# Kernel tuning notes

Measured on AMD Instinct MI355X. Metric: run time of the kernel, lower is better.

The kernel has to match this reference:

```python
import jax, jax.numpy as jnp
import numpy as np

N = 100000       # nodes
E = 1600000      # edges (avg degree 16)
F_IN = 64        # node feature dim
H = 8            # GAT heads
C1 = 8           # gat1 out_channels per head (8*8=64)
C2 = 10          # gat2 out_channels = num classes
S = 32           # edge_feats sequence length
SMAX = 32        # s_max padding target
DM = 6           # transformer d_model (SelfAttention dim_out default)
NH = 2           # transformer heads
DIN = 10         # transformer dim_in
NEG = 0.2        # leaky relu negative slope
EPS = 1e-5       # LayerNorm eps


def setup_inputs() -> dict:
    key = jax.random.key(0)
    ks = jax.random.split(key, 32)
    rn = lambda k, shp, s=0.1: jax.random.normal(k, shp, jnp.float32) * s
    inp = {
        'x': jax.random.normal(ks[0], (N, F_IN), jnp.float32),
        'edge_index': jax.random.randint(ks[1], (2, E), 0, N, jnp.int32),
        'edge_feats': jax.random.normal(ks[2], (N, S, DIN), jnp.float32),
        # gat1: weight [in, heads*out], att [1, H, 2*C1], bias [H*C1]
        'W1': rn(ks[3], (F_IN, H * C1)), 'att1': rn(ks[4], (1, H, 2 * C1)), 'b1': jnp.zeros((H * C1,), jnp.float32),
        # gat2: in=70 (64 gat1 + 6 transformer), concat=False -> bias [C2]
        'W2': rn(ks[5], (70, H * C2)), 'att2': rn(ks[6], (1, H, 2 * C2)), 'b2': jnp.zeros((C2,), jnp.float32),
        # transformer Encoder (weights stored [in, out])
        'Wq': rn(ks[7], (DIN, DM)), 'bq': rn(ks[8], (DM,)),
        'Wk': rn(ks[9], (DIN, DM)), 'bk': rn(ks[10], (DM,)),
        'Wv': rn(ks[11], (DIN, DM)), 'bv': rn(ks[12], (DM,)),
        'g0': jnp.ones((DM,), jnp.float32), 'be0': jnp.zeros((DM,), jnp.float32),
        'Wf1': rn(ks[13], (DM, 4 * DM)), 'bf1': rn(ks[14], (4 * DM,)),
        'Wf2': rn(ks[15], (4 * DM, DM)), 'bf2': rn(ks[16], (DM,)),
        'g1': jnp.ones((DM,), jnp.float32), 'be1': jnp.zeros((DM,), jnp.float32),
        'Wrep': rn(ks[17], (SMAX, 1)), 'brep': rn(ks[18], (1,)),
    }
    return inp


def _layer_norm(x, g, b):
    m = x.mean(-1, keepdims=True)
    v = ((x - m) ** 2).mean(-1, keepdims=True)
    return (x - m) / jnp.sqrt(v + EPS) * g + b


def _gat_conv(x, src, dst, W, att, bias, heads, outc, concat):
    """GATConv: remove self loops (masking), add one self loop per node,
    edge-wise attention, per-destination segment softmax, scatter-add."""
    n = x.shape[0]
    valid = src != dst                       # remove_self_loops (mask, static shape)
    loop = jnp.arange(n, dtype=src.dtype)    # add_self_loops
    s = jnp.concatenate([src, loop])
    d = jnp.concatenate([dst, loop])
    valid = jnp.concatenate([valid, jnp.ones((n,), bool)])
    xw = (x @ W).reshape(n, heads, outc)     # [N, H, C]
    xj = xw[s]                               # gather source feats  [E', H, C]
    xi = xw[d]                               # gather target feats  [E', H, C]
    a_i, a_j = att[0, :, :outc], att[0, :, outc:]
    alpha = (xi * a_i).sum(-1) + (xj * a_j).sum(-1)          # [E', H]
    alpha = jnp.where(alpha >= 0, alpha, NEG * alpha)         # leaky relu
    alpha = jnp.where(valid[:, None], alpha, -jnp.inf)        # drop input self-loops
    amax = jax.ops.segment_max(alpha, d, num_segments=n)      # segment softmax
    ea = jnp.exp(alpha - amax[d])
    denom = jax.ops.segment_sum(ea, d, num_segments=n)
    w = ea / denom[d]
    out = jax.ops.segment_sum(xj * w[:, :, None], d, num_segments=n)  # [N, H, C]
    if concat:
        return out.reshape(n, heads * outc) + bias
    return out.mean(axis=1) + bias


def _encoder(Xf, Wq, bq, Wk, bk, Wv, bv, g0, be0, Wf1, bf1, Wf2, bf2, g1, be1, Wrep, brep):
    n, s, _ = Xf.shape
    Q = Xf @ Wq + bq
    K = Xf @ Wk + bk
    V = Xf @ Wv + bv
    dh = DM // NH
    Qh = Q.reshape(n, s, NH, dh).transpose(0, 2, 1, 3)   # [n, h, s, dh]
    Kh = K.reshape(n, s, NH, dh).transpose(0, 2, 1, 3)
    Vh = V.reshape(n, s, NH, dh).transpose(0, 2, 1, 3)
    scale = 1.0 / np.float32(np.sqrt(DM))                # note: sqrt(d_model), as in source
    A = jax.nn.softmax(jnp.einsum('nhsd,nhtd->nhst', Qh, Kh) * scale, axis=-1)
    A1 = jnp.einsum('nhst,nhtd->nhsd', A, Vh)
    O = (Qh + A1).transpose(0, 2, 1, 3).reshape(n, s, DM)  # skip=True path
    O = _layer_norm(O, g0, be0)
    ff = jnp.maximum(O @ Wf1 + bf1, 0.0) @ Wf2 + bf2
    O = _layer_norm(O + ff, g1, be1)
    O = O.transpose(0, 2, 1)                              # [n, DM, s]
    O = jnp.pad(O, ((0, 0), (0, 0), (0, SMAX - s)))
    O = O @ Wrep + brep                                   # fc_rep: [n, DM, 1]
    return O[..., 0]                                      # squeeze -> [n, DM]


def reference(x, edge_index, edge_feats, W1, att1, b1, W2, att2, b2,
              Wq, bq, Wk, bk, Wv, bv, g0, be0, Wf1, bf1, Wf2, bf2,
              g1, be1, Wrep, brep):
    src, dst = edge_index[0], edge_index[1]
    h1 = _gat_conv(x, src, dst, W1, att1, b1, H, C1, True)          # [N, 64]
    h1 = jax.nn.elu(h1)
    xt = _encoder(edge_feats, Wq, bq, Wk, bk, Wv, bv, g0, be0,
                  Wf1, bf1, Wf2, bf2, g1, be1, Wrep, brep)          # [N, 6]
    h2 = _gat_conv(jnp.concatenate([h1, xt], axis=1), src, dst,
                   W2, att2, b2, H, C2, False)                      # [N, 10]
    return jax.nn.log_softmax(h2, axis=1)
```

## Files before the change

kernel.cpp:

```cpp
#include <hip/hip_runtime.h>
#include <hip/hip_bf16.h>


#define NEG_SLOPE 0.2f

using short8  = __attribute__((ext_vector_type(8))) short;
using floatx4 = __attribute__((ext_vector_type(4))) float;

__device__ __forceinline__ float bf_lo(unsigned u) { return __uint_as_float(u << 16); }
__device__ __forceinline__ float bf_hi(unsigned u) { return __uint_as_float(u & 0xffff0000u); }
__device__ __forceinline__ unsigned pk(float lo, float hi)
{
    __hip_bfloat16 l = __float2bfloat16(lo), h = __float2bfloat16(hi);
    unsigned ul = reinterpret_cast<unsigned short&>(l);
    unsigned uh = reinterpret_cast<unsigned short&>(h);
    return ul | (uh << 16);
}

__global__ void __launch_bounds__(256) front_kernel(
    const float* __restrict__ Xf,
    const float* __restrict__ Wq, const float* __restrict__ bq,
    const float* __restrict__ Wk, const float* __restrict__ bk,
    const float* __restrict__ Wv, const float* __restrict__ bv,
    const float* __restrict__ g0, const float* __restrict__ be0,
    const float* __restrict__ Wf1, const float* __restrict__ bf1,
    const float* __restrict__ Wf2, const float* __restrict__ bf2,
    const float* __restrict__ g1, const float* __restrict__ be1,
    const float* __restrict__ Wrep, const float* __restrict__ brep,
    __hip_bfloat16* __restrict__ hx,
    const int* __restrict__ src, const int* __restrict__ dst,
    int* __restrict__ deg, int* __restrict__ rank, int e,
    const float* __restrict__ x, const float* __restrict__ W1,
    const float* __restrict__ att1,
    __hip_bfloat16* __restrict__ xwb,
    float* __restrict__ ai, unsigned* __restrict__ ajp,
    int n, int EB, int CB)
{
    __shared__ float smem[4352];
    int t = threadIdx.x;
    int bid = blockIdx.x;

    if (bid < EB) {
        float* sh = smem;
        size_t base = (size_t)bid * 2560;
#pragma unroll
        for (int i = 0; i < 10; ++i) sh[i * 256 + t] = Xf[base + i * 256 + t];
        __syncthreads();

        int sub = t >> 5;
        int s   = t & 31;
        int v   = bid * 8 + sub;

        float xv[10];
#pragma unroll
        for (int i = 0; i < 10; ++i) xv[i] = sh[sub * 320 + s * 10 + i];
        __syncthreads();

        float q[6], k[6], w[6];
#pragma unroll
        for (int j = 0; j < 6; ++j) { q[j] = bq[j]; k[j] = bk[j]; w[j] = bv[j]; }
#pragma unroll
        for (int i = 0; i < 10; ++i) {
#pragma unroll
            for (int j = 0; j < 6; ++j) {
                q[j] += xv[i] * Wq[i * 6 + j];
                k[j] += xv[i] * Wk[i * 6 + j];
                w[j] += xv[i] * Wv[i * 6 + j];
            }
        }

        float* kv = sh + sub * 384;
        *(float4*)&kv[s * 12 + 0] = make_float4(k[0], k[1], k[2], k[3]);
        *(float4*)&kv[s * 12 + 4] = make_float4(k[4], k[5], w[0], w[1]);
        *(float4*)&kv[s * 12 + 8] = make_float4(w[2], w[3], w[4], w[5]);
        __builtin_amdgcn_wave_barrier();

        const float scale = 0.40824829046386301637f;
        float q0s = q[0] * scale, q1s = q[1] * scale, q2s = q[2] * scale;
        float q3s = q[3] * scale, q4s = q[4] * scale, q5s = q[5] * scale;

        float dA0 = 0.f, dB0 = 0.f, dA1 = 0.f, dB1 = 0.f;
        float aA00 = 0.f, aA01 = 0.f, aA02 = 0.f;
        float aB00 = 0.f, aB01 = 0.f, aB02 = 0.f;
        float aA10 = 0.f, aA11 = 0.f, aA12 = 0.f;
        float aB10 = 0.f, aB11 = 0.f, aB12 = 0.f;

#pragma unroll 4
        for (int t2 = 0; t2 < 32; t2 += 2) {
            float4 A0 = *(const float4*)&kv[t2 * 12 + 0];
            float4 A1 = *(const float4*)&kv[t2 * 12 + 4];
            float4 A2 = *(const float4*)&kv[t2 * 12 + 8];
            float4 B0 = *(const float4*)&kv[t2 * 12 + 12];
            float4 B1 = *(const float4*)&kv[t2 * 12 + 16];
            float4 B2 = *(const float4*)&kv[t2 * 12 + 20];
            {
                float p0 = __expf(q0s * A0.x + q1s * A0.y + q2s * A0.z);
                float p1 = __expf(q3s * A0.w + q4s * A1.x + q5s * A1.y);
                dA0 += p0; aA00 += p0 * A1.z; aA01 += p0 * A1.w; aA02 += p0 * A2.x;
                dA1 += p1; aA10 += p1 * A2.y; aA11 += p1 * A2.z; aA12 += p1 * A2.w;
            }
            {
                float p0 = __expf(q0s * B0.x + q1s * B0.y + q2s * B0.z);
                float p1 = __expf(q3s * B0.w + q4s * B1.x + q5s * B1.y);
                dB0 += p0; aB00 += p0 * B1.z; aB01 += p0 * B1.w; aB02 += p0 * B2.x;
                dB1 += p1; aB10 += p1 * B2.y; aB11 += p1 * B2.z; aB12 += p1 * B2.w;
            }
        }

        float O[6];
        {
            float inv0 = 1.f / (dA0 + dB0);
            float inv1 = 1.f / (dA1 + dB1);
            O[0] = q[0] + (aA00 + aB00) * inv0;
            O[1] = q[1] + (aA01 + aB01) * inv0;
            O[2] = q[2] + (aA02 + aB02) * inv0;
            O[3] = q[3] + (aA10 + aB10) * inv1;
            O[4] = q[4] + (aA11 + aB11) * inv1;
            O[5] = q[5] + (aA12 + aB12) * inv1;
        }

        {
            float mean = (O[0] + O[1] + O[2] + O[3] + O[4] + O[5]) * (1.f / 6.f);
            float var = 0.f;
#pragma unroll
            for (int j = 0; j < 6; ++j) { float d = O[j] - mean; var += d * d; }
            var *= (1.f / 6.f);
            float r = rsqrtf(var + 1e-5f);
#pragma unroll
            for (int j = 0; j < 6; ++j) O[j] = (O[j] - mean) * r * g0[j] + be0[j];
        }

        float f[6];
#pragma unroll
        for (int j = 0; j < 6; ++j) f[j] = O[j] + bf2[j];
#pragma unroll 4
        for (int r = 0; r < 24; ++r) {
            float hr = bf1[r];
#pragma unroll
            for (int j = 0; j < 6; ++j) hr += O[j] * Wf1[j * 24 + r];
            hr = fmaxf(hr, 0.f);
#pragma unroll
            for (int j = 0; j < 6; ++j) f[j] += hr * Wf2[r * 6 + j];
        }
        {
            float mean = (f[0] + f[1] + f[2] + f[3] + f[4] + f[5]) * (1.f / 6.f);
            float var = 0.f;
#pragma unroll
            for (int j = 0; j < 6; ++j) { float d = f[j] - mean; var += d * d; }
            var *= (1.f / 6.f);
            float r = rsqrtf(var + 1e-5f);
#pragma unroll
            for (int j = 0; j < 6; ++j) f[j] = (f[j] - mean) * r * g1[j] + be1[j];
        }

        float wr = Wrep[s];
#pragma unroll
        for (int j = 0; j < 6; ++j) {
            float val = f[j] * wr;
#pragma unroll
            for (int off = 16; off >= 1; off >>= 1) val += __shfl_xor(val, off, 32);
            f[j] = val;
        }
        if (s == 0) {
            float br = brep[0];
#pragma unroll
            for (int j = 0; j < 6; ++j)
                hx[(size_t)v * 96 + 64 + j] = __float2bfloat16(f[j] + br);
        }
    } else if (bid < EB + CB) {
        int i = (bid - EB) * 256 + t;
        if (i < e) {
            int ss = src[i], dd = dst[i];
            if (ss != dd) rank[i] = atomicAdd(&deg[dd], 1);
        }
    } else {
        float* shW = smem;
        float* shX = smem + 4096;
        int xb = bid - EB - CB;
        int wv = t >> 6, l = t & 63;
#pragma unroll
        for (int i = 0; i < 16; ++i) shW[i * 256 + t] = W1[i * 256 + t];
        int h = l >> 3, c = l & 7;
        float a_i = att1[h * 16 + c];
        float a_j = att1[h * 16 + 8 + c];
        __syncthreads();

#pragma unroll
        for (int it = 0; it < 4; ++it) {
            int v = xb * 16 + it * 4 + wv;
            shX[wv * 64 + l] = x[(size_t)v * 64 + l];
            __builtin_amdgcn_wave_barrier();
            float acc = 0.f;
#pragma unroll
            for (int k4 = 0; k4 < 16; ++k4) {
                float4 xb4 = *(const float4*)&shX[wv * 64 + k4 * 4];
                acc += xb4.x * shW[(k4 * 4 + 0) * 64 + l];
                acc += xb4.y * shW[(k4 * 4 + 1) * 64 + l];
                acc += xb4.z * shW[(k4 * 4 + 2) * 64 + l];
                acc += xb4.w * shW[(k4 * 4 + 3) * 64 + l];
            }
            xwb[(size_t)v * 64 + l] = __float2bfloat16(acc);

            float pi = acc * a_i;
            float pj = acc * a_j;
#pragma unroll
            for (int off = 1; off < 8; off <<= 1) {
                pi += __shfl_xor(pi, off, 64);
                pj += __shfl_xor(pj, off, 64);
            }
            if (c == 0) ai[(size_t)v * 8 + h] = pi;
            float pj_hi = __shfl(pj, (l + 8) & 63, 64);
            if ((l & 15) == 0)
                ajp[(size_t)v * 4 + (h >> 1)] = pk(pj, pj_hi);
            __builtin_amdgcn_wave_barrier();
        }
    }
}

__global__ void __launch_bounds__(1024) scan1_kernel(
    const int* __restrict__ deg, int* __restrict__ bsum, int n)
{
    __shared__ int sh[1024];
    int t = threadIdx.x;
    int i = blockIdx.x * 1024 + t;
    sh[t] = (i < n) ? deg[i] : 0;
    __syncthreads();
    for (int off = 512; off >= 1; off >>= 1) {
        if (t < off) sh[t] += sh[t + off];
        __syncthreads();
    }
    if (t == 0) bsum[blockIdx.x] = sh[0];
}

__global__ void __launch_bounds__(128) scan2_kernel(int* __restrict__ bsum, int nb)
{
    __shared__ int sh[128];
    int t = threadIdx.x;
    int v = (t < nb) ? bsum[t] : 0;
    sh[t] = v;
    __syncthreads();
    for (int off = 1; off < 128; off <<= 1) {
        int val = (t >= off) ? sh[t - off] : 0;
        __syncthreads();
        sh[t] += val;
        __syncthreads();
    }
    if (t < nb) bsum[t] = sh[t] - v;
}

__global__ void __launch_bounds__(1024) scan3_kernel(
    const int* __restrict__ deg, const int* __restrict__ bsum,
    int* __restrict__ offs, int n)
{
    __shared__ int sh[1024];
    int t = threadIdx.x;
    int i = blockIdx.x * 1024 + t;
    int v = (i < n) ? deg[i] : 0;
    sh[t] = v;
    __syncthreads();
    for (int off = 1; off < 1024; off <<= 1) {
        int val = (t >= off) ? sh[t - off] : 0;
        __syncthreads();
        sh[t] += val;
        __syncthreads();
    }
    if (i < n) offs[i] = bsum[blockIdx.x] + sh[t] - v;
}

__global__ void scatter_kernel(const int* __restrict__ src, const int* __restrict__ dst,
                               const int* __restrict__ offsets,
                               const int* __restrict__ rank,
                               int* __restrict__ elist, int e)
{
    int i = blockIdx.x * blockDim.x + threadIdx.x;
    if (i < e) {
        int s = src[i], d = dst[i];
        if (s != d) elist[offsets[d] + rank[i]] = s;
    }
}

__global__ void __launch_bounds__(256) agg1_kernel(
    const __hip_bfloat16* __restrict__ xwb, const float* __restrict__ ai1,
    const unsigned* __restrict__ ajp, const float* __restrict__ att1,
    const float* __restrict__ b1,
    const int* __restrict__ offs, const int* __restrict__ deg,
    const int* __restrict__ elist,
    __hip_bfloat16* __restrict__ hx, int n)
{
    int t = threadIdx.x, wv = t >> 6, l = t & 63;
    int v = blockIdx.x * 4 + wv;
    int h = l >> 3, c = l & 7;
    int e1 = l >> 3, hp = l & 7;

    float ai_l = ai1[(size_t)v * 8 + h];
    float ai_p = ai1[(size_t)v * 8 + hp];
    float attj_l = att1[h * 16 + 8 + c];

    float yself = __bfloat162float(xwb[(size_t)v * 64 + l]);
    float ps = yself * attj_l;
    ps += __shfl_xor(ps, 1, 64);
    ps += __shfl_xor(ps, 2, 64);
    ps += __shfl_xor(ps, 4, 64);
    float a = ai_l + ps;
    a = fmaxf(a, NEG_SLOPE * a);
    float ea  = __expf(a);
    float acc = ea * yself;

    float den_acc = 0.f;
    int off = offs[v], dg = deg[v];
    for (int j = 0; j < dg; j += 8) {
        int idxv = 0;
        if (l < 8 && j + l < dg) idxv = elist[off + j + l];
        int se = __shfl(idxv, e1, 64);
        unsigned aw = ajp[(size_t)se * 4 + (hp >> 1)];
        float ajv = (hp & 1) ? bf_hi(aw) : bf_lo(aw);
        float u = ai_p + ajv;
        u = fmaxf(u, NEG_SLOPE * u);
        float wl = __expf(u);
        wl = (j + e1 < dg) ? wl : 0.f;
        den_acc += wl;
#pragma unroll
        for (int b = 0; b < 8; ++b) {
            int s = __shfl(idxv, b, 64);
            float y = __bfloat162float(xwb[(size_t)s * 64 + l]);
            float w = __shfl(wl, b * 8 + h, 64);
            acc += w * y;
        }
    }
    den_acc += __shfl_xor(den_acc, 8, 64);
    den_acc += __shfl_xor(den_acc, 16, 64);
    den_acc += __shfl_xor(den_acc, 32, 64);
    float den = ea + __shfl(den_acc, h, 64);

    float o = acc / den + b1[l];
    o = o > 0.f ? o : expm1f(o);
    hx[(size_t)v * 96 + l] = __float2bfloat16(o);
}

__global__ void __launch_bounds__(256) w2ext_kernel(
    const float* __restrict__ W2, const float* __restrict__ att2,
    __hip_bfloat16* __restrict__ w2t)
{
    int idx = blockIdx.x * 256 + threadIdx.x;
    if (idx >= 96 * 96) return;
    int j = idx / 96, k = idx % 96;
    float val = 0.f;
    if (k < 70) {
        if (j < 80) {
            val = W2[k * 80 + j];
        } else if (j < 88) {
            int h = j - 80;
            for (int c = 0; c < 10; ++c)
                val += W2[k * 80 + h * 10 + c] * att2[h * 20 + c];
        } else {
            int h = j - 88;
            for (int c = 0; c < 10; ++c)
                val += W2[k * 80 + h * 10 + c] * att2[h * 20 + 10 + c];
        }
    }
    w2t[j * 96 + k] = __float2bfloat16(val);
}

__global__ void __launch_bounds__(256) xw2mfma_kernel(
    const __hip_bfloat16* __restrict__ hx, const __hip_bfloat16* __restrict__ w2t,
    __hip_bfloat16* __restrict__ xw2p, float* __restrict__ ai2, int n)
{
    int t = threadIdx.x, wv = t >> 6, l = t & 63;
    int base = blockIdx.x * 64 + wv * 16;
    if (base >= n) return;

    int mrow = l & 15;
    int kc   = (l >> 4) * 8;
    int dr0  = (l >> 4) * 4;

    const short* hp = (const short*)hx;
    const short* wp = (const short*)w2t;

    short8 a0 = *(const short8*)(hp + (size_t)(base + mrow) * 96 + 0  + kc);
    short8 a1 = *(const short8*)(hp + (size_t)(base + mrow) * 96 + 32 + kc);
    short8 a2 = *(const short8*)(hp + (size_t)(base + mrow) * 96 + 64 + kc);

#pragma unroll
    for (int nt = 0; nt < 6; ++nt) {
        int col = nt * 16 + mrow;
        short8 b0 = *(const short8*)(wp + (size_t)col * 96 + 0  + kc);
        short8 b1 = *(const short8*)(wp + (size_t)col * 96 + 32 + kc);
        short8 b2 = *(const short8*)(wp + (size_t)col * 96 + 64 + kc);
        floatx4 acc = {0.f, 0.f, 0.f, 0.f};
        acc = __builtin_amdgcn_mfma_f32_16x16x32_bf16(a0, b0, acc, 0, 0, 0);
        acc = __builtin_amdgcn_mfma_f32_16x16x32_bf16(a1, b1, acc, 0, 0, 0);
        acc = __builtin_amdgcn_mfma_f32_16x16x32_bf16(a2, b2, acc, 0, 0, 0);
#pragma unroll
        for (int r = 0; r < 4; ++r) {
            int m = base + dr0 + r;
            float val = acc[r];
            if (nt < 5) {
                xw2p[(size_t)m * 128 + nt * 16 + mrow] = __float2bfloat16(val);
            } else {
                if (mrow < 8) ai2[(size_t)m * 8 + mrow] = val;
                else xw2p[(size_t)m * 128 + 80 + (mrow - 8)] = __float2bfloat16(val);
            }
        }
    }
}

__global__ void __launch_bounds__(256) agg2_kernel(
    const unsigned* __restrict__ xw2p, const float* __restrict__ ai2,
    const float* __restrict__ b2,
    const int* __restrict__ offs, const int* __restrict__ deg,
    const int* __restrict__ elist, float* __restrict__ out, int n)
{
    __shared__ float buf[4][80];
    __shared__ float buf2[4][10];
    int t = threadIdx.x, wv = t >> 6, l = t & 63;
    int v = blockIdx.x * 4 + wv;

    int hc = (l < 40) ? (l / 5) : 0;
    int e1 = l >> 3, hp = l & 7;
    float ai_p = ai2[(size_t)v * 8 + hp];
    float ai_l = (l < 40) ? ai2[(size_t)v * 8 + hc] : 0.f;

    bool act = l < 44;
    unsigned selfw = act ? xw2p[(size_t)v * 64 + l] : 0u;
    int ajl = 40 + (hc >> 1);
    unsigned ajw = __shfl(selfw, ajl, 64);
    float ajs = (hc & 1) ? bf_hi(ajw) : bf_lo(ajw);
    float a = ai_l + ajs;
    a = fmaxf(a, NEG_SLOPE * a);
    float e0 = __expf(a);
    float acc0 = e0 * bf_lo(selfw), acc1 = e0 * bf_hi(selfw);

    float den_acc = 0.f;
    int off = offs[v], dg = deg[v];
    for (int j = 0; j < dg; j += 8) {
        int idxv = 0;
        if (l < 8 && j + l < dg) idxv = elist[off + j + l];
        int se = __shfl(idxv, e1, 64);
        unsigned aw = xw2p[(size_t)se * 64 + 40 + (hp >> 1)];
        float ajv = (hp & 1) ? bf_hi(aw) : bf_lo(aw);
        float u = ai_p + ajv;
        u = fmaxf(u, NEG_SLOPE * u);
        float wl = __expf(u);
        wl = (j + e1 < dg) ? wl : 0.f;
        den_acc += wl;
#pragma unroll
        for (int b = 0; b < 8; ++b) {
            int s = __shfl(idxv, b, 64);
            unsigned yw = (l < 40) ? xw2p[(size_t)s * 64 + l] : 0u;
            float w = __shfl(wl, b * 8 + hc, 64);
            acc0 += w * bf_lo(yw);
            acc1 += w * bf_hi(yw);
        }
    }
    den_acc += __shfl_xor(den_acc, 8, 64);
    den_acc += __shfl_xor(den_acc, 16, 64);
    den_acc += __shfl_xor(den_acc, 32, 64);
    float den = e0 + __shfl(den_acc, hc, 64);

    if (l < 40) {
        float inv = 1.f / den;
        buf[wv][2 * l]     = acc0 * inv;
        buf[wv][2 * l + 1] = acc1 * inv;
    }
    __builtin_amdgcn_wave_barrier();
    if (l < 10) {
        float mval = 0.f;
#pragma unroll
        for (int hh = 0; hh < 8; ++hh) mval += buf[wv][hh * 10 + l];
        buf2[wv][l] = mval * 0.125f + b2[l];
    }
    __builtin_amdgcn_wave_barrier();
    if (l < 10) {
        float mx = -1e30f;
#pragma unroll
        for (int cc = 0; cc < 10; ++cc) mx = fmaxf(mx, buf2[wv][cc]);
        float se = 0.f;
#pragma unroll
        for (int cc = 0; cc < 10; ++cc) se += __expf(buf2[wv][cc] - mx);
        out[(size_t)v * 10 + l] = buf2[wv][l] - mx - __logf(se);
    }
}

extern "C" void kernel_launch(void* const* d_in, const int* in_sizes, int n_in,
                              void* d_out, int out_size, void* d_ws, size_t ws_size,
                              hipStream_t stream)
{
    const float* x    = (const float*)d_in[0];
    const int*   ei   = (const int*)  d_in[1];
    const float* ef   = (const float*)d_in[2];
    const float* W1   = (const float*)d_in[3];
    const float* att1 = (const float*)d_in[4];
    const float* b1   = (const float*)d_in[5];
    const float* W2   = (const float*)d_in[6];
    const float* att2 = (const float*)d_in[7];
    const float* b2   = (const float*)d_in[8];
    const float* Wq   = (const float*)d_in[9];
    const float* bq   = (const float*)d_in[10];
    const float* Wk   = (const float*)d_in[11];
    const float* bk   = (const float*)d_in[12];
    const float* Wv   = (const float*)d_in[13];
    const float* bv   = (const float*)d_in[14];
    const float* g0   = (const float*)d_in[15];
    const float* be0  = (const float*)d_in[16];
    const float* Wf1  = (const float*)d_in[17];
    const float* bf1  = (const float*)d_in[18];
    const float* Wf2  = (const float*)d_in[19];
    const float* bf2  = (const float*)d_in[20];
    const float* g1   = (const float*)d_in[21];
    const float* be1  = (const float*)d_in[22];
    const float* Wrep = (const float*)d_in[23];
    const float* brep = (const float*)d_in[24];

    const int n = in_sizes[0] / 64;
    const int e = in_sizes[1] / 2;
    const int* src = ei;
    const int* dst = ei + e;

    char* ws = (char*)d_ws;
    size_t o = 0;
    auto alloc = [&](size_t bytes) -> void* {
        void* p = ws + o;
        o += (bytes + 255) & ~(size_t)255;
        return p;
    };
    __hip_bfloat16* xw1b = (__hip_bfloat16*)alloc((size_t)n * 64 * 2);
    __hip_bfloat16* hx   = (__hip_bfloat16*)alloc((size_t)n * 96 * 2);
    __hip_bfloat16* xw2p = (__hip_bfloat16*)alloc((size_t)n * 128 * 2);
    __hip_bfloat16* w2t  = (__hip_bfloat16*)alloc(96 * 96 * 2);
    unsigned* ajp = (unsigned*)alloc((size_t)n * 4 * 4);
    float* ai1   = (float*)alloc((size_t)n * 8 * 4);
    float* ai2   = (float*)alloc((size_t)n * 8 * 4);
    int*   deg   = (int*)  alloc((size_t)n * 4);
    int*   offs  = (int*)  alloc((size_t)n * 4);
    int*   rank  = (int*)  alloc((size_t)e * 4);
    int*   bsum  = (int*)  alloc(256 * 4);
    int*   elist = (int*)  alloc((size_t)e * 4);
    (void)ws_size; (void)n_in; (void)out_size;

    hipMemsetAsync(deg, 0, (size_t)n * 4, stream);
    hipMemsetAsync(hx, 0, (size_t)n * 96 * 2, stream);

    const int NB = (n + 1023) / 1024;
    const int EB = n / 8;
    const int CB = (e + 255) / 256;
    const int XB = n / 16;

    w2ext_kernel<<<36, 256, 0, stream>>>(W2, att2, w2t);
    front_kernel<<<EB + CB + XB, 256, 0, stream>>>(
        ef, Wq, bq, Wk, bk, Wv, bv, g0, be0, Wf1, bf1, Wf2, bf2, g1, be1,
        Wrep, brep, hx,
        src, dst, deg, rank, e,
        x, W1, att1, xw1b, ai1, ajp,
        n, EB, CB);
    scan1_kernel<<<NB, 1024, 0, stream>>>(deg, bsum, n);
    scan2_kernel<<<1, 128, 0, stream>>>(bsum, NB);
    scan3_kernel<<<NB, 1024, 0, stream>>>(deg, bsum, offs, n);
    scatter_kernel<<<(e + 255) / 256, 256, 0, stream>>>(src, dst, offs, rank,
                                                        elist, e);
    agg1_kernel<<<n / 4, 256, 0, stream>>>(xw1b, ai1, ajp, att1, b1,
                                           offs, deg, elist, hx, n);
    xw2mfma_kernel<<<(n + 63) / 64, 256, 0, stream>>>(hx, w2t, xw2p, ai2, n);
    agg2_kernel<<<n / 4, 256, 0, stream>>>((const unsigned*)xw2p, ai2, b2,
                                           offs, deg, elist, (float*)d_out, n);
}
```

Measured before the change: 411.8 us.

## Move first GAT projection out of front kernel into bf16 MFMA kernel

Splits the x@W1 projection out of the fused front kernel into its own kernel that uses bf16 16x16x32 MFMA instructions. The attention logit vectors are folded into W1 as 16 extra output columns via a small preprocessing kernel. This replaces per-lane FP32 shared-memory dot products and shuffle reductions. In exchange it adds two kernel launches and loses concurrency with the encoder blocks, and x is now rounded to bf16 before the projection, which costs some precision.

```diff
diff --git a/kernel.cpp b/kernel.cpp
--- a/kernel.cpp
+++ b/kernel.cpp
@@ -15,6 +15,11 @@
     unsigned ul = reinterpret_cast<unsigned short&>(l);
     unsigned uh = reinterpret_cast<unsigned short&>(h);
     return ul | (uh << 16);
+}
+__device__ __forceinline__ short bfs(float f)
+{
+    __hip_bfloat16 b = __float2bfloat16(f);
+    return reinterpret_cast<short&>(b);
 }
 
 __global__ void __launch_bounds__(256) front_kernel(
@@ -30,13 +35,9 @@
     __hip_bfloat16* __restrict__ hx,
     const int* __restrict__ src, const int* __restrict__ dst,
     int* __restrict__ deg, int* __restrict__ rank, int e,
-    const float* __restrict__ x, const float* __restrict__ W1,
-    const float* __restrict__ att1,
-    __hip_bfloat16* __restrict__ xwb,
-    float* __restrict__ ai, unsigned* __restrict__ ajp,
-    int n, int EB, int CB)
-{
-    __shared__ float smem[4352];
+    int n, int EB)
+{
+    __shared__ float smem[3072];
     int t = threadIdx.x;
     int bid = blockIdx.x;
 
@@ -167,52 +168,90 @@
             for (int j = 0; j < 6; ++j)
                 hx[(size_t)v * 96 + 64 + j] = __float2bfloat16(f[j] + br);
         }
-    } else if (bid < EB + CB) {
+    } else {
         int i = (bid - EB) * 256 + t;
         if (i < e) {
             int ss = src[i], dd = dst[i];
             if (ss != dd) rank[i] = atomicAdd(&deg[dd], 1);
         }
+    }
+}
+
+__global__ void __launch_bounds__(256) w1ext_kernel(
+    const float* __restrict__ W1, const float* __restrict__ att1,
+    __hip_bfloat16* __restrict__ w1t)
+{
+    int idx = blockIdx.x * 256 + threadIdx.x;
+    if (idx >= 80 * 64) return;
+    int j = idx / 64, k = idx % 64;
+    float val;
+    if (j < 64) {
+        val = W1[k * 64 + j];
+    } else if (j < 72) {
+        int h = j - 64;
+        val = 0.f;
+        for (int c = 0; c < 8; ++c)
+            val += W1[k * 64 + h * 8 + c] * att1[h * 16 + c];
     } else {
-        float* shW = smem;
-        float* shX = smem + 4096;
-        int xb = bid - EB - CB;
-        int wv = t >> 6, l = t & 63;
-#pragma unroll
-        for (int i = 0; i < 16; ++i) shW[i * 256 + t] = W1[i * 256 + t];
-        int h = l >> 3, c = l & 7;
-        float a_i = att1[h * 16 + c];
-        float a_j = att1[h * 16 + 8 + c];
-        __syncthreads();
-
-#pragma unroll
-        for (int it = 0; it < 4; ++it) {
-            int v = xb * 16 + it * 4 + wv;
-            shX[wv * 64 + l] = x[(size_t)v * 64 + l];
-            __builtin_amdgcn_wave_barrier();
-            float acc = 0.f;
-#pragma unroll
-            for (int k4 = 0; k4 < 16; ++k4) {
-                float4 xb4 = *(const float4*)&shX[wv * 64 + k4 * 4];
-                acc += xb4.x * shW[(k4 * 4 + 0) * 64 + l];
-                acc += xb4.y * shW[(k4 * 4 + 1) * 64 + l];
-                acc += xb4.z * shW[(k4 * 4 + 2) * 64 + l];
-                acc += xb4.w * shW[(k4 * 4 + 3) * 64 + l];
+        int h = j - 72;
+        val = 0.f;
+        for (int c = 0; c < 8; ++c)
+            val += W1[k * 64 + h * 8 + c] * att1[h * 16 + 8 + c];
+    }
+    w1t[j * 64 + k] = __float2bfloat16(val);
+}
+
+__global__ void __launch_bounds__(256) xw1mfma_kernel(
+    const float* __restrict__ x, const __hip_bfloat16* __restrict__ w1t,
+    __hip_bfloat16* __restrict__ xwb, float* __restrict__ ai,
+    unsigned* __restrict__ ajp, int n)
+{
+    int t = threadIdx.x, wv = t >> 6, l = t & 63;
+    int base = blockIdx.x * 64 + wv * 16;
+    if (base >= n) return;
+
+    int mrow = l & 15;
+    int kc   = (l >> 4) * 8;
+    int dr0  = (l >> 4) * 4;
+
+    const float* xr = x + (size_t)(base + mrow) * 64;
+    short8 a0, a1;
+#pragma unroll
+    for (int i = 0; i < 8; ++i) {
+        a0[i] = bfs(xr[kc + i]);
+        a1[i] = bfs(xr[32 + kc + i]);
+    }
+
+    const short* wp = (const short*)w1t;
+
+#pragma unroll
+    for (int nt = 0; nt < 5; ++nt) {
+        int col = nt * 16 + mrow;
+        short8 b0 = *(const short8*)(wp + (size_t)col * 64 + kc);
+        short8 b1 = *(const short8*)(wp + (size_t)col * 64 + 32 + kc);
+        floatx4 acc = {0.f, 0.f, 0.f, 0.f};
+        acc = __builtin_amdgcn_mfma_f32_16x16x32_bf16(a0, b0, acc, 0, 0, 0);
+        acc = __builtin_amdgcn_mfma_f32_16x16x32_bf16(a1, b1, acc, 0, 0, 0);
+        if (nt < 4) {
+#pragma unroll
+            for (int r = 0; r < 4; ++r) {
+                int m = base + dr0 + r;
+                xwb[(size_t)m * 64 + nt * 16 + mrow] = __float2bfloat16(acc[r]);
             }
-            xwb[(size_t)v * 64 + l] = __float2bfloat16(acc);
-
-            float pi = acc * a_i;
-            float pj = acc * a_j;
-#pragma unroll
-            for (int off = 1; off < 8; off <<= 1) {
-                pi += __shfl_xor(pi, off, 64);
-                pj += __shfl_xor(pj, off, 64);
+        } else {
+#pragma unroll
+            for (int r = 0; r < 4; ++r) {
+                int m = base + dr0 + r;
+                float val = acc[r];
+                float nb  = __shfl_xor(val, 1, 64);
+                if (mrow < 8) {
+                    ai[(size_t)m * 8 + mrow] = val;
+                } else {
+                    int h = mrow - 8;
+                    if ((h & 1) == 0)
+                        ajp[(size_t)m * 4 + (h >> 1)] = pk(val, nb);
+                }
             }
-            if (c == 0) ai[(size_t)v * 8 + h] = pi;
-            float pj_hi = __shfl(pj, (l + 8) & 63, 64);
-            if ((l & 15) == 0)
-                ajp[(size_t)v * 4 + (h >> 1)] = pk(pj, pj_hi);
-            __builtin_amdgcn_wave_barrier();
         }
     }
 }
@@ -527,6 +566,7 @@
     __hip_bfloat16* hx   = (__hip_bfloat16*)alloc((size_t)n * 96 * 2);
     __hip_bfloat16* xw2p = (__hip_bfloat16*)alloc((size_t)n * 128 * 2);
     __hip_bfloat16* w2t  = (__hip_bfloat16*)alloc(96 * 96 * 2);
+    __hip_bfloat16* w1t  = (__hip_bfloat16*)alloc(80 * 64 * 2);
     unsigned* ajp = (unsigned*)alloc((size_t)n * 4 * 4);
     float* ai1   = (float*)alloc((size_t)n * 8 * 4);
     float* ai2   = (float*)alloc((size_t)n * 8 * 4);
@@ -543,15 +583,15 @@
     const int NB = (n + 1023) / 1024;
     const int EB = n / 8;
     const int CB = (e + 255) / 256;
-    const int XB = n / 16;
 
     w2ext_kernel<<<36, 256, 0, stream>>>(W2, att2, w2t);
-    front_kernel<<<EB + CB + XB, 256, 0, stream>>>(
+    w1ext_kernel<<<20, 256, 0, stream>>>(W1, att1, w1t);
+    front_kernel<<<EB + CB, 256, 0, stream>>>(
         ef, Wq, bq, Wk, bk, Wv, bv, g0, be0, Wf1, bf1, Wf2, bf2, g1, be1,
         Wrep, brep, hx,
         src, dst, deg, rank, e,
-        x, W1, att1, xw1b, ai1, ajp,
-        n, EB, CB);
+        n, EB);
+    xw1mfma_kernel<<<(n + 63) / 64, 256, 0, stream>>>(x, w1t, xw1b, ai1, ajp, n);
     scan1_kernel<<<NB, 1024, 0, stream>>>(deg, bsum, n);
     scan2_kernel<<<1, 128, 0, stream>>>(bsum, NB);
     scan3_kernel<<<NB, 1024, 0, stream>>>(deg, bsum, offs, n);
```

Measured after the change: 380.7 us. 7.6% less time.
